# Kernel tuning notes

Measured on AMD Instinct MI355X. Metric: run time of the kernel, lower is better.

Reference implementation:

```python
import jax, jax.numpy as jnp
import numpy as np

N = 100000
E = 1600000
F_IN = 100
HID = 128
CLS = 47


def _glorot(key, shape):
    fan_in, fan_out = shape[1], shape[0]
    lim = (6.0 / (fan_in + fan_out)) ** 0.5
    return jax.random.uniform(key, shape, jnp.float32, -lim, lim)


def setup_inputs() -> dict:
    key = jax.random.key(0)
    ks = jax.random.split(key, 12)
    x0 = jax.random.normal(ks[0], (N, F_IN), jnp.float32)
    edge_index = jax.random.randint(ks[1], (2, E), 0, N, jnp.int32)
    edge_weight = jax.random.uniform(ks[2], (E,), jnp.float32)
    params = {
        'W1_rel': _glorot(ks[3], (HID, F_IN)),
        'W1_root': _glorot(ks[4], (HID, F_IN)),
        'b1': jnp.zeros((HID,), jnp.float32),
        'W2_rel': _glorot(ks[5], (HID, HID)),
        'W2_root': _glorot(ks[6], (HID, HID)),
        'b2': jnp.zeros((HID,), jnp.float32),
        'W3_rel': _glorot(ks[7], (HID, HID)),
        'W3_root': _glorot(ks[8], (HID, HID)),
        'b3': jnp.zeros((HID,), jnp.float32),
        'W_lin': _glorot(ks[9], (CLS, 3 * HID)),
        'b_lin': jnp.zeros((CLS,), jnp.float32),
    }
    return dict(x0=x0, edge_index=edge_index, edge_weight=edge_weight, **params)


def _graph_conv(x, src, dst, ew, W_rel, W_root, b):
    # gather source features, scale by edge weight, scatter-add to destinations
    msg = x[src] * ew[:, None]                       # [E, d]
    agg = jax.ops.segment_sum(msg, dst, num_segments=N)  # [N, d]
    return agg @ W_rel.T + x @ W_root.T + b


def reference(x0, edge_index, edge_weight,
              W1_rel, W1_root, b1,
              W2_rel, W2_root, b2,
              W3_rel, W3_root, b3,
              W_lin, b_lin):
    src, dst = edge_index[0], edge_index[1]
    x1 = jax.nn.relu(_graph_conv(x0, src, dst, edge_weight, W1_rel, W1_root, b1))
    x2 = jax.nn.relu(_graph_conv(x1, src, dst, edge_weight, W2_rel, W2_root, b2))
    x3 = jax.nn.relu(_graph_conv(x2, src, dst, edge_weight, W3_rel, W3_root, b3))
    x = jnp.concatenate([x1, x2, x3], axis=-1)       # [N, 3*HID]
    logits = x @ W_lin.T + b_lin                     # [N, CLS]
    return jax.nn.log_softmax(logits, axis=-1)
```

## Files before the change

### kernel.cpp

```cpp
#include <hip/hip_runtime.h>
#include <hip/hip_bf16.h>
#include <stdint.h>

#define NN 100000
#define NE 1600000
#define FIN 100
#define HID 128
#define CLS 47
#define NBUK 391

typedef __attribute__((ext_vector_type(8))) short bf16x8;
typedef __attribute__((ext_vector_type(4))) float f32x4;
typedef __attribute__((ext_vector_type(2))) float f32x2;

#define AS1(p) ((const __attribute__((address_space(1))) void*)(p))
#define AS3(p) ((__attribute__((address_space(3))) void*)(p))

__device__ __forceinline__ uint16_t f2bf(float f) {
  union { float f; uint32_t u; } v; v.f = f;
  uint32_t r = v.u + 0x7fffu + ((v.u >> 16) & 1u);
  return (uint16_t)(r >> 16);
}

__global__ void pack_weights(const float* __restrict__ W1r, const float* __restrict__ W1o,
                             const float* __restrict__ W2r, const float* __restrict__ W2o,
                             const float* __restrict__ W3r, const float* __restrict__ W3o,
                             uint16_t* __restrict__ B1, uint16_t* __restrict__ B2, uint16_t* __restrict__ B3) {
  int idx = blockIdx.x * 256 + threadIdx.x;
  int l = idx >> 15;
  int rem = idx & 32767;
  int j = rem >> 8;
  int k = rem & 255;
  if (l == 0) {
    uint16_t v = 0;
    if (k < FIN) v = f2bf(W1r[j*FIN + k]);
    else if (k >= 128 && k < 128 + FIN) v = f2bf(W1o[j*FIN + (k - 128)]);
    B1[j*256 + k] = v;
  } else if (l == 1) {
    B2[j*256 + k] = (k < 128) ? f2bf(W2r[j*128 + k]) : f2bf(W2o[j*128 + (k - 128)]);
  } else {
    B3[j*256 + k] = (k < 128) ? f2bf(W3r[j*128 + k]) : f2bf(W3o[j*128 + (k - 128)]);
  }
}

__global__ void pack_wl(const float* __restrict__ Wl, uint16_t* __restrict__ Wlb) {
  int idx = blockIdx.x * 256 + threadIdx.x;
  int r = idx / 384;
  int c = idx - r * 384;
  Wlb[idx] = (r < CLS) ? f2bf(Wl[r*384 + c]) : (uint16_t)0;
}

__global__ __launch_bounds__(256) void pad_x0(const float* __restrict__ x0, uint16_t* __restrict__ x0p,
                                              uint8_t* __restrict__ x0f8) {
  int n = blockIdx.x * 4 + (threadIdx.x >> 6);
  int c = 2 * (threadIdx.x & 63);
  uint32_t o = 0;
  uint16_t o8 = 0;
  if (c < FIN) {
    float2 v = *(const float2*)(x0 + (size_t)n*FIN + c);
    o = ((uint32_t)f2bf(v.y) << 16) | (uint32_t)f2bf(v.x);
    o8 = (uint16_t)__builtin_amdgcn_cvt_pk_fp8_f32(v.x, v.y, 0, false);
  }
  *(uint32_t*)(x0p + (size_t)n*HID + c) = o;
  *(uint16_t*)(x0f8 + (size_t)n*128 + c) = o8;
}

__global__ __launch_bounds__(512) void bucket_hist(const int* __restrict__ dst, int* __restrict__ bcnt) {
  __shared__ int h[NBUK];
  int tid = threadIdx.x;
  for (int i = tid; i < NBUK; i += 512) h[i] = 0;
  __syncthreads();
  int tile0 = blockIdx.x * 8192;
  int n = NE - tile0; if (n > 8192) n = 8192;
  for (int i = tid; i < n; i += 512) atomicAdd(&h[dst[tile0 + i] >> 8], 1);
  __syncthreads();
  for (int i = tid; i < NBUK; i += 512) if (h[i]) atomicAdd(&bcnt[i], h[i]);
}

__global__ __launch_bounds__(512) void bucket_scan(const int* __restrict__ bcnt,
                                                   int* __restrict__ bfill, int* __restrict__ bbase) {
  __shared__ int sh[512];
  int t = threadIdx.x;
  int v = (t < NBUK) ? bcnt[t] : 0;
  sh[t] = v;
  __syncthreads();
  for (int off = 1; off < 512; off <<= 1) {
    int tv = (t >= off) ? sh[t - off] : 0;
    __syncthreads();
    sh[t] += tv;
    __syncthreads();
  }
  if (t < NBUK) {
    int e = sh[t] - v;
    bfill[t] = e;
    bbase[t] = e;
  }
  if (t == 0) bbase[NBUK] = NE;
}

__global__ __launch_bounds__(512) void binscat(const int* __restrict__ src, const int* __restrict__ dst,
                                               const float* __restrict__ ew,
                                               int* __restrict__ bfill, int2* __restrict__ ebin) {
  __shared__ int h[NBUK];
  __shared__ int base[NBUK];
  int tid = threadIdx.x;
  for (int i = tid; i < NBUK; i += 512) h[i] = 0;
  __syncthreads();
  int tile0 = blockIdx.x * 8192;
  int n = NE - tile0; if (n > 8192) n = 8192;
  for (int i = tid; i < n; i += 512) atomicAdd(&h[dst[tile0 + i] >> 8], 1);
  __syncthreads();
  for (int i = tid; i < NBUK; i += 512) base[i] = h[i] ? atomicAdd(&bfill[i], h[i]) : 0;
  __syncthreads();
  for (int i = tid; i < NBUK; i += 512) h[i] = 0;
  __syncthreads();
  for (int i = tid; i < n; i += 512) {
    int e = tile0 + i;
    int d = dst[e];
    int b = d >> 8;
    int r = atomicAdd(&h[b], 1);
    ebin[base[b] + r] = make_int2(src[e] | ((d & 255) << 17), __float_as_int(ew[e]));
  }
}

__global__ __launch_bounds__(256) void bucket_csr(const int2* __restrict__ ebin,
                                                  const int* __restrict__ bbase,
                                                  int* __restrict__ row_start,
                                                  int2* __restrict__ erec) {
  __shared__ int sh[256];
  __shared__ int fill[256];
  int b = blockIdx.x;
  int tid = threadIdx.x;
  int ebase = bbase[b], eend = bbase[b + 1];
  int cnt = eend - ebase;
  sh[tid] = 0;
  __syncthreads();
  for (int i = tid; i < cnt; i += 256) atomicAdd(&sh[(uint32_t)ebin[ebase + i].x >> 17], 1);
  __syncthreads();
  int histv = sh[tid];
  __syncthreads();
  for (int off = 1; off < 256; off <<= 1) {
    int tv = (tid >= off) ? sh[tid - off] : 0;
    __syncthreads();
    sh[tid] += tv;
    __syncthreads();
  }
  int excl = sh[tid] - histv;
  int node = b * 256 + tid;
  if (node <= NN) row_start[node] = ebase + excl;
  fill[tid] = ebase + excl;
  __syncthreads();
  for (int i = tid; i < cnt; i += 256) {
    int2 rec = ebin[ebase + i];
    int dl = (uint32_t)rec.x >> 17;
    int s = rec.x & 0x1FFFF;
    int pos = atomicAdd(&fill[dl], 1);
    erec[pos] = make_int2(s << 7, rec.y);
  }
}

__global__ __launch_bounds__(256) void spmm_kernel(const uint8_t* __restrict__ x8,
                                                   const int* __restrict__ row_start,
                                                   const int2* __restrict__ erec,
                                                   uint16_t* __restrict__ agg) {
  int wave = threadIdx.x >> 6;
  int l = threadIdx.x & 63;
  int half = l >> 5, li = l & 31;
  int n = blockIdx.x * 8 + wave * 2 + half;
  int s0 = row_start[n], s1 = row_start[n + 1];
  const char* xb = (const char*)x8;
  int loff = 4 * li;
  float a0 = 0.f, a1 = 0.f, a2 = 0.f, a3 = 0.f;
  const int2* ep = erec + s0;
  for (int e0 = s0; e0 < s1; e0 += 16, ep += 16) {
    int2 r[16];
    #pragma unroll
    for (int u = 0; u < 16; ++u) r[u] = ep[u];
    uint32_t g[16];
    #pragma unroll
    for (int u = 0; u < 16; ++u)
      g[u] = *(const uint32_t*)(xb + (size_t)(uint32_t)(r[u].x + loff));
    #pragma unroll
    for (int u = 0; u < 16; ++u) {
      float w = (e0 + u < s1) ? __int_as_float(r[u].y) : 0.f;
      f32x2 lo = __builtin_amdgcn_cvt_pk_f32_fp8(g[u], false);
      f32x2 hi = __builtin_amdgcn_cvt_pk_f32_fp8(g[u], true);
      a0 += w * lo[0]; a1 += w * lo[1]; a2 += w * hi[0]; a3 += w * hi[1];
    }
  }
  uint2 o;
  o.x = ((uint32_t)f2bf(a1) << 16) | (uint32_t)f2bf(a0);
  o.y = ((uint32_t)f2bf(a3) << 16) | (uint32_t)f2bf(a2);
  *(uint2*)(agg + (size_t)n*HID + 4*li) = o;
}

__global__ __launch_bounds__(256) void gemm_kernel(const uint16_t* __restrict__ A1, const uint16_t* __restrict__ A2,
                                                   const uint16_t* __restrict__ Bm, const float* __restrict__ bias,
                                                   uint16_t* __restrict__ out, uint8_t* __restrict__ out8) {
  __shared__ uint16_t ldsA[128 * 32];
  __shared__ uint16_t ldsB[128 * 32];
  int t = threadIdx.x;
  int n0 = blockIdx.x * 128;
  int lane = t & 63, wave = t >> 6;
  int wm = (wave >> 1) * 64, wn = (wave & 1) * 64;
  int l15 = lane & 15, quad = lane >> 4;

  f32x4 acc[4][4];
  #pragma unroll
  for (int i = 0; i < 4; ++i)
    #pragma unroll
    for (int j = 0; j < 4; ++j) acc[i][j] = (f32x4){0.f, 0.f, 0.f, 0.f};

  for (int kt = 0; kt < 8; ++kt) {
    int kbase = kt * 32;
    const uint16_t* Asrc = (kbase < 128) ? A1 : A2;
    int klocal = kbase & 127;
    #pragma unroll
    for (int q = 0; q < 2; ++q) {
      int u = t + q * 256;
      int r = u >> 2;
      int kg = (u & 3) * 8;
      int rowA = n0 + r; if (rowA >= NN) rowA = NN - 1;
      __builtin_amdgcn_global_load_lds(AS1(Asrc + (size_t)rowA*HID + klocal + kg), AS3(&ldsA[u * 8]), 16, 0, 0);
      __builtin_amdgcn_global_load_lds(AS1(Bm + r*256 + kbase + kg), AS3(&ldsB[u * 8]), 16, 0, 0);
    }
    __syncthreads();
    bf16x8 af[4], bfr[4];
    #pragma unroll
    for (int mi = 0; mi < 4; ++mi) af[mi] = *(const bf16x8*)&ldsA[(wm + mi*16 + l15) * 32 + quad * 8];
    #pragma unroll
    for (int ni = 0; ni < 4; ++ni) bfr[ni] = *(const bf16x8*)&ldsB[(wn + ni*16 + l15) * 32 + quad * 8];
    #pragma unroll
    for (int mi = 0; mi < 4; ++mi)
      #pragma unroll
      for (int ni = 0; ni < 4; ++ni)
        acc[mi][ni] = __builtin_amdgcn_mfma_f32_16x16x32_bf16(af[mi], bfr[ni], acc[mi][ni], 0, 0, 0);
    __syncthreads();
  }

  #pragma unroll
  for (int mi = 0; mi < 4; ++mi) {
    #pragma unroll
    for (int ni = 0; ni < 4; ++ni) {
      int c = wn + ni*16 + l15;
      float bc = bias[c];
      #pragma unroll
      for (int i = 0; i < 4; ++i) {
        int r = n0 + wm + mi*16 + quad*4 + i;
        if (r < NN) {
          float v = acc[mi][ni][i] + bc;
          v = v > 0.f ? v : 0.f;
          out[(size_t)r*HID + c] = f2bf(v);
          if (out8) out8[(size_t)r*128 + c] = (uint8_t)__builtin_amdgcn_cvt_pk_fp8_f32(v, v, 0, false);
        }
      }
    }
  }
}

__global__ __launch_bounds__(256) void final_kernel(const uint16_t* __restrict__ x1, const uint16_t* __restrict__ x2,
                                                    const uint16_t* __restrict__ x3,
                                                    const uint16_t* __restrict__ Wlb, const float* __restrict__ bl,
                                                    float* __restrict__ out) {
  __shared__ uint16_t ldsA[4 * 64 * 8];
  __shared__ uint16_t ldsW[4 * 64 * 8];
  int t = threadIdx.x;
  int lane = t & 63, wave = t >> 6;
  int n0 = blockIdx.x * 64;
  int l15 = lane & 15, quad = lane >> 4;

  int sc2 = t >> 6, sr = t & 63;
  int rowA = n0 + sr; if (rowA >= NN) rowA = NN - 1;
  int rowW = sr < 48 ? sr : 47;

  f32x4 acc[3];
  #pragma unroll
  for (int i = 0; i < 3; ++i) acc[i] = (f32x4){0.f, 0.f, 0.f, 0.f};

  #pragma unroll
  for (int kt = 0; kt < 12; ++kt) {
    const uint16_t* xs = (kt < 4) ? x1 : (kt < 8) ? x2 : x3;
    int klocal = (kt & 3) * 32 + sc2 * 8;
    __builtin_amdgcn_global_load_lds(AS1(xs + (size_t)rowA*HID + klocal), AS3(&ldsA[t * 8]), 16, 0, 0);
    __builtin_amdgcn_global_load_lds(AS1(Wlb + (size_t)rowW*384 + kt*32 + sc2*8), AS3(&ldsW[t * 8]), 16, 0, 0);
    __syncthreads();
    bf16x8 af = *(const bf16x8*)&ldsA[(quad * 64 + wave * 16 + l15) * 8];
    #pragma unroll
    for (int nt = 0; nt < 3; ++nt) {
      bf16x8 wf = *(const bf16x8*)&ldsW[(quad * 64 + nt * 16 + l15) * 8];
      acc[nt] = __builtin_amdgcn_mfma_f32_16x16x32_bf16(af, wf, acc[nt], 0, 0, 0);
    }
    __syncthreads();
  }

  int nb = n0 + wave * 16;
  float bias[3]; bool valid[3];
  #pragma unroll
  for (int nt = 0; nt < 3; ++nt) {
    int c = nt*16 + l15;
    valid[nt] = (c < CLS);
    bias[nt] = valid[nt] ? bl[c] : 0.f;
  }

  #pragma unroll
  for (int i = 0; i < 4; ++i) {
    int r = nb + quad*4 + i;
    float v0 = acc[0][i] + bias[0];
    float v1 = acc[1][i] + bias[1];
    float v2 = valid[2] ? (acc[2][i] + bias[2]) : -INFINITY;
    float m = fmaxf(v0, fmaxf(v1, v2));
    #pragma unroll
    for (int off = 8; off >= 1; off >>= 1) m = fmaxf(m, __shfl_xor(m, off, 64));
    float s = __expf(v0 - m) + __expf(v1 - m) + (valid[2] ? __expf(v2 - m) : 0.f);
    #pragma unroll
    for (int off = 8; off >= 1; off >>= 1) s += __shfl_xor(s, off, 64);
    float lse = m + __logf(s);
    if (r < NN) {
      out[(size_t)r*CLS + l15]      = v0 - lse;
      out[(size_t)r*CLS + 16 + l15] = v1 - lse;
      if (valid[2]) out[(size_t)r*CLS + 32 + l15] = v2 - lse;
    }
  }
}

extern "C" void kernel_launch(void* const* d_in, const int* in_sizes, int n_in,
                              void* d_out, int out_size, void* d_ws, size_t ws_size,
                              hipStream_t stream) {
  (void)in_sizes; (void)n_in; (void)out_size; (void)ws_size;
  const float* x0  = (const float*)d_in[0];
  const int*   ei  = (const int*)d_in[1];
  const float* ew  = (const float*)d_in[2];
  const float* W1r = (const float*)d_in[3];
  const float* W1o = (const float*)d_in[4];
  const float* b1  = (const float*)d_in[5];
  const float* W2r = (const float*)d_in[6];
  const float* W2o = (const float*)d_in[7];
  const float* b2  = (const float*)d_in[8];
  const float* W3r = (const float*)d_in[9];
  const float* W3o = (const float*)d_in[10];
  const float* b3  = (const float*)d_in[11];
  const float* Wl  = (const float*)d_in[12];
  const float* bl  = (const float*)d_in[13];
  const int* src = ei;
  const int* dst = ei + NE;

  char* ws = (char*)d_ws;
  size_t off = 0;
  auto alloc = [&](size_t bytes) -> void* {
    void* p = ws + off;
    off += (bytes + 255) & ~(size_t)255;
    return p;
  };
  uint16_t* x0p = (uint16_t*)alloc((size_t)NN * HID * 2);
  uint16_t* xb1 = (uint16_t*)alloc((size_t)NN * HID * 2);
  uint16_t* xb3 = (uint16_t*)alloc((size_t)NN * HID * 2);
  uint16_t* agg = (uint16_t*)alloc((size_t)NN * HID * 2);
  int2*   erec      = (int2*)alloc((size_t)(NE + 16) * 8);
  int2*   ebin      = (int2*)alloc((size_t)NE * 8);
  int*    row_start = (int*)alloc((size_t)(NN + 1) * 4);
  int*    bcnt      = (int*)alloc(NBUK * 4);
  int*    bfill     = (int*)alloc(NBUK * 4);
  int*    bbase     = (int*)alloc((NBUK + 1) * 4);
  uint16_t* B1 = (uint16_t*)alloc(128 * 256 * 2);
  uint16_t* B2 = (uint16_t*)alloc(128 * 256 * 2);
  uint16_t* B3 = (uint16_t*)alloc(128 * 256 * 2);
  uint16_t* Wlb = (uint16_t*)alloc(48 * 384 * 2);
  uint8_t* x0f8  = (uint8_t*)alloc((size_t)NN * 128);
  uint8_t* xb2f8 = (uint8_t*)alloc((size_t)NN * 128);
  uint16_t* xb2 = x0p;
  uint8_t* xb1f8 = (uint8_t*)ebin;

  const int TB = (NE + 8191) / 8192;

  hipMemsetAsync(bcnt, 0, NBUK * 4, stream);
  hipMemsetAsync(erec + NE, 0, 16 * sizeof(int2), stream);
  pack_weights<<<384, 256, 0, stream>>>(W1r, W1o, W2r, W2o, W3r, W3o, B1, B2, B3);
  pack_wl<<<72, 256, 0, stream>>>(Wl, Wlb);
  pad_x0<<<NN / 4, 256, 0, stream>>>(x0, x0p, x0f8);
  bucket_hist<<<TB, 512, 0, stream>>>(dst, bcnt);
  bucket_scan<<<1, 512, 0, stream>>>(bcnt, bfill, bbase);
  binscat<<<TB, 512, 0, stream>>>(src, dst, ew, bfill, ebin);
  bucket_csr<<<NBUK, 256, 0, stream>>>(ebin, bbase, row_start, erec);

  spmm_kernel<<<NN / 8, 256, 0, stream>>>(x0f8, row_start, erec, agg);
  gemm_kernel<<<(NN + 127) / 128, 256, 0, stream>>>(agg, x0p, B1, b1, xb1, xb1f8);
  spmm_kernel<<<NN / 8, 256, 0, stream>>>(xb1f8, row_start, erec, agg);
  gemm_kernel<<<(NN + 127) / 128, 256, 0, stream>>>(agg, xb1, B2, b2, xb2, xb2f8);
  spmm_kernel<<<NN / 8, 256, 0, stream>>>(xb2f8, row_start, erec, agg);
  gemm_kernel<<<(NN + 127) / 128, 256, 0, stream>>>(agg, xb2, B3, b3, xb3, nullptr);

  final_kernel<<<(NN + 63) / 64, 256, 0, stream>>>(xb1, xb2, xb3, Wlb, bl, (float*)d_out);
}
```

Baseline: 414.5 us.

## Peel SpMM tail, pack FMAs, and use k-chunk-major LDS layout in GEMM

The SpMM loop now handles full 16-edge chunks without a per-edge bounds check, processes the remainder in a separate peeled iteration, and accumulates in float2 vectors so the compiler can emit packed FMAs. The GEMM changes its LDS tile to a k-chunk-major layout and doubles the K step to 64, which halves the number of barrier pairs. The new layout is meant to remove LDS bank conflicts on the 16-byte fragment reads. The cost is larger LDS tiles per block and some duplicated code for the tail.

```diff
diff --git a/kernel.cpp b/kernel.cpp
--- a/kernel.cpp
+++ b/kernel.cpp
@@ -170,9 +170,12 @@
   int s0 = row_start[n], s1 = row_start[n + 1];
   const char* xb = (const char*)x8;
   int loff = 4 * li;
-  float a0 = 0.f, a1 = 0.f, a2 = 0.f, a3 = 0.f;
+  f32x2 a01 = (f32x2){0.f, 0.f}, a23 = (f32x2){0.f, 0.f};
   const int2* ep = erec + s0;
-  for (int e0 = s0; e0 < s1; e0 += 16, ep += 16) {
+  int deg = s1 - s0;
+  int nfull = deg & ~15;
+  const int2* epf = ep + nfull;
+  for (; ep < epf; ep += 16) {
     int2 r[16];
     #pragma unroll
     for (int u = 0; u < 16; ++u) r[u] = ep[u];
@@ -182,23 +185,40 @@
       g[u] = *(const uint32_t*)(xb + (size_t)(uint32_t)(r[u].x + loff));
     #pragma unroll
     for (int u = 0; u < 16; ++u) {
-      float w = (e0 + u < s1) ? __int_as_float(r[u].y) : 0.f;
-      f32x2 lo = __builtin_amdgcn_cvt_pk_f32_fp8(g[u], false);
-      f32x2 hi = __builtin_amdgcn_cvt_pk_f32_fp8(g[u], true);
-      a0 += w * lo[0]; a1 += w * lo[1]; a2 += w * hi[0]; a3 += w * hi[1];
+      float w = __int_as_float(r[u].y);
+      f32x2 w2 = (f32x2){w, w};
+      a01 += w2 * __builtin_amdgcn_cvt_pk_f32_fp8(g[u], false);
+      a23 += w2 * __builtin_amdgcn_cvt_pk_f32_fp8(g[u], true);
+    }
+  }
+  int rem = deg - nfull;
+  if (rem) {
+    int2 r[16];
+    #pragma unroll
+    for (int u = 0; u < 16; ++u) r[u] = ep[u];
+    uint32_t g[16];
+    #pragma unroll
+    for (int u = 0; u < 16; ++u)
+      g[u] = *(const uint32_t*)(xb + (size_t)(uint32_t)(r[u].x + loff));
+    #pragma unroll
+    for (int u = 0; u < 16; ++u) {
+      float w = (u < rem) ? __int_as_float(r[u].y) : 0.f;
+      f32x2 w2 = (f32x2){w, w};
+      a01 += w2 * __builtin_amdgcn_cvt_pk_f32_fp8(g[u], false);
+      a23 += w2 * __builtin_amdgcn_cvt_pk_f32_fp8(g[u], true);
     }
   }
   uint2 o;
-  o.x = ((uint32_t)f2bf(a1) << 16) | (uint32_t)f2bf(a0);
-  o.y = ((uint32_t)f2bf(a3) << 16) | (uint32_t)f2bf(a2);
+  o.x = ((uint32_t)f2bf(a01[1]) << 16) | (uint32_t)f2bf(a01[0]);
+  o.y = ((uint32_t)f2bf(a23[1]) << 16) | (uint32_t)f2bf(a23[0]);
   *(uint2*)(agg + (size_t)n*HID + 4*li) = o;
 }
 
 __global__ __launch_bounds__(256) void gemm_kernel(const uint16_t* __restrict__ A1, const uint16_t* __restrict__ A2,
                                                    const uint16_t* __restrict__ Bm, const float* __restrict__ bias,
                                                    uint16_t* __restrict__ out, uint8_t* __restrict__ out8) {
-  __shared__ uint16_t ldsA[128 * 32];
-  __shared__ uint16_t ldsB[128 * 32];
+  __shared__ uint16_t ldsA[8 * 128 * 8];
+  __shared__ uint16_t ldsB[8 * 128 * 8];
   int t = threadIdx.x;
   int n0 = blockIdx.x * 128;
   int lane = t & 63, wave = t >> 6;
@@ -211,30 +231,33 @@
     #pragma unroll
     for (int j = 0; j < 4; ++j) acc[i][j] = (f32x4){0.f, 0.f, 0.f, 0.f};
 
-  for (int kt = 0; kt < 8; ++kt) {
-    int kbase = kt * 32;
+  for (int kt = 0; kt < 4; ++kt) {
+    int kbase = kt * 64;
     const uint16_t* Asrc = (kbase < 128) ? A1 : A2;
     int klocal = kbase & 127;
     #pragma unroll
-    for (int q = 0; q < 2; ++q) {
+    for (int q = 0; q < 4; ++q) {
       int u = t + q * 256;
-      int r = u >> 2;
-      int kg = (u & 3) * 8;
+      int kc = u >> 7, r = u & 127;
       int rowA = n0 + r; if (rowA >= NN) rowA = NN - 1;
-      __builtin_amdgcn_global_load_lds(AS1(Asrc + (size_t)rowA*HID + klocal + kg), AS3(&ldsA[u * 8]), 16, 0, 0);
-      __builtin_amdgcn_global_load_lds(AS1(Bm + r*256 + kbase + kg), AS3(&ldsB[u * 8]), 16, 0, 0);
-    }
-    __syncthreads();
-    bf16x8 af[4], bfr[4];
-    #pragma unroll
-    for (int mi = 0; mi < 4; ++mi) af[mi] = *(const bf16x8*)&ldsA[(wm + mi*16 + l15) * 32 + quad * 8];
-    #pragma unroll
-    for (int ni = 0; ni < 4; ++ni) bfr[ni] = *(const bf16x8*)&ldsB[(wn + ni*16 + l15) * 32 + quad * 8];
-    #pragma unroll
-    for (int mi = 0; mi < 4; ++mi)
+      __builtin_amdgcn_global_load_lds(AS1(Asrc + (size_t)rowA*HID + klocal + kc*8), AS3(&ldsA[u * 8]), 16, 0, 0);
+      __builtin_amdgcn_global_load_lds(AS1(Bm + r*256 + kbase + kc*8), AS3(&ldsB[u * 8]), 16, 0, 0);
+    }
+    __syncthreads();
+    #pragma unroll
+    for (int ks = 0; ks < 2; ++ks) {
+      int kc = ks * 4 + quad;
+      bf16x8 af[4], bfr[4];
       #pragma unroll
-      for (int ni = 0; ni < 4; ++ni)
-        acc[mi][ni] = __builtin_amdgcn_mfma_f32_16x16x32_bf16(af[mi], bfr[ni], acc[mi][ni], 0, 0, 0);
+      for (int mi = 0; mi < 4; ++mi) af[mi] = *(const bf16x8*)&ldsA[(kc * 128 + wm + mi*16 + l15) * 8];
+      #pragma unroll
+      for (int ni = 0; ni < 4; ++ni) bfr[ni] = *(const bf16x8*)&ldsB[(kc * 128 + wn + ni*16 + l15) * 8];
+      #pragma unroll
+      for (int mi = 0; mi < 4; ++mi)
+        #pragma unroll
+        for (int ni = 0; ni < 4; ++ni)
+          acc[mi][ni] = __builtin_amdgcn_mfma_f32_16x16x32_bf16(af[mi], bfr[ni], acc[mi][ni], 0, 0, 0);
+    }
     __syncthreads();
   }
 
```

Result: slower. 434.0 us (+4.7%).
